# Kernel optimization log

Hardware: AMD Instinct MI355X
Metric: run time of the kernel (lower is better)

## Reference

```python
import jax, jax.numpy as jnp
import numpy as np
import math


def _instance_cl(z1, z2):
    # z1, z2: [B, T, C] -> per-element instance contrastive loss [B, T]
    B = z1.shape[0]
    z = jnp.concatenate([z1, z2], axis=0)          # [2B, T, C]
    z = z.transpose(1, 0, 2)                        # [T, 2B, C]
    sim = jnp.einsum('tic,tjc->tij', z, z)          # [T, 2B, 2B]
    # drop diagonal: tril(-1) shifted + triu(1) shifted -> [T, 2B, 2B-1]
    logits = jnp.tril(sim, -1)[:, :, :-1] + jnp.triu(sim, 1)[:, :, 1:]
    logits = -jax.nn.log_softmax(logits, axis=-1)
    i = jnp.arange(B)
    loss = (logits[:, i, B + i - 1] + logits[:, B + i, i]) / 2.0   # [T, B]
    return loss.T                                    # [B, T]


def _temporal_cl(z1, z2):
    # z1, z2: [B, T, C] -> per-timestep temporal contrastive loss [B, T]
    T = z1.shape[1]
    z = jnp.concatenate([z1, z2], axis=1)            # [B, 2T, C]
    sim = jnp.einsum('bic,bjc->bij', z, z)           # [B, 2T, 2T]
    logits = jnp.tril(sim, -1)[:, :, :-1] + jnp.triu(sim, 1)[:, :, 1:]
    logits = -jax.nn.log_softmax(logits, axis=-1)
    t = jnp.arange(T)
    return (logits[:, t, T + t - 1] + logits[:, T + t, t]) / 2.0   # [B, T]


def _contrastive_corr(z1, z2, alpha=0.5):
    # per-(batch, timestep) contrastive score, shape [B, L]
    return alpha * _instance_cl(z1, z2) + (1.0 - alpha) * _temporal_cl(z1, z2)


def setup_inputs() -> dict:
    key = jax.random.key(0)
    k1, k2, k3 = jax.random.split(key, 3)
    B, L, H, E = 4, 2048, 8, 64
    queries = jax.random.normal(k1, (B, L, H, E), dtype=jnp.float32)
    keys = jax.random.normal(k2, (B, L, H, E), dtype=jnp.float32)
    values = jax.random.normal(k3, (B, L, H, E), dtype=jnp.float32)
    attn_mask = jnp.zeros((1,), dtype=bool)  # unused; ProbMask is rebuilt internally
    return {"queries": queries, "keys": keys, "values": values, "attn_mask": attn_mask}


FACTOR = 1.0


def reference(queries, keys, values, attn_mask):
    B, L, H, E = queries.shape
    # S == L here so key/value slicing branch is a no-op
    corr = _contrastive_corr(queries.reshape(B, L, H * E),
                             keys.reshape(B, L, H * E))       # [B, L]
    top_k = int(FACTOR * math.log(L))                          # static (=7 for L=2048)
    _, index = jax.lax.top_k(corr.mean(axis=0), top_k)         # [K]
    corr_top = corr[:, index]                                  # [B, K]
    # scores[b,h,k,l] = corr_top[b,k] broadcast over h and l
    scores = jnp.broadcast_to(corr_top[:, None, :, None], (B, H, top_k, L))
    # ProbMask: mask future positions l > index[k] (causal for the selected queries)
    mask = jnp.arange(L)[None, :] > index[:, None]             # [K, L]
    scores = jnp.where(mask[None, None, :, :], -jnp.inf, scores)
    attn = jax.nn.softmax(scores, axis=-1)                     # [B, H, K, L]
    V = values.transpose(0, 2, 1, 3)                           # [B, H, L, D]
    context = jnp.cumsum(V, axis=2)                            # initial context (mask_flag=True)
    out = jnp.einsum('bhkl,bhld->bhkd', attn, V)               # [B, H, K, D]
    context = context.at[:, :, index, :].set(out)              # scatter update
    return context
```

## Files before the change

### kernel.cpp

```cpp
#include <hip/hip_runtime.h>
#include <math.h>


typedef __attribute__((ext_vector_type(8))) short short8;
typedef __attribute__((ext_vector_type(8))) unsigned short ushort8;
typedef __attribute__((ext_vector_type(4))) float f32x4;

typedef const __attribute__((address_space(1))) void* gas_ptr;
typedef __attribute__((address_space(3))) void* las_ptr;

#define EXP_OFF 80.0f

__device__ __forceinline__ void async_cp16(const void* g, void* l) {
  __builtin_amdgcn_global_load_lds((gas_ptr)g, (las_ptr)l, 16, 0, 0);
}

__device__ __forceinline__ unsigned short f2bf(float x) {
  union { float f; unsigned int u; } v; v.f = x;
  unsigned int r = v.u + 0x7FFFu + ((v.u >> 16) & 1u);
  return (unsigned short)(r >> 16);
}

__global__ __launch_bounds__(256) void convert_bf16_kernel(
    const float* __restrict__ Q, const float* __restrict__ K,
    unsigned short* __restrict__ Z) {
  int tid = blockIdx.x * 256 + threadIdx.x;
  int row = tid >> 6;
  int c0 = (tid & 63) * 8;
  int b = row >> 12, i = row & 4095;
  const float* src = (i < 2048)
      ? Q + ((size_t)(b * 2048 + i) * 512 + c0)
      : K + ((size_t)(b * 2048 + (i - 2048)) * 512 + c0);
  float4 v0 = ((const float4*)src)[0];
  float4 v1 = ((const float4*)src)[1];
  ushort8 o;
  o[0] = f2bf(v0.x); o[1] = f2bf(v0.y); o[2] = f2bf(v0.z); o[3] = f2bf(v0.w);
  o[4] = f2bf(v1.x); o[5] = f2bf(v1.y); o[6] = f2bf(v1.z); o[7] = f2bf(v1.w);
  *(ushort8*)(Z + (size_t)row * 512 + c0) = o;
}

__global__ __launch_bounds__(256, 3) void temporal_gemm_kernel(
    const unsigned short* __restrict__ Z, float* __restrict__ part,
    float* __restrict__ lse_inst ,
    float* __restrict__ posdot ) {
  __shared__ __align__(16) unsigned short As[2][128 * 32];
  __shared__ __align__(16) unsigned short Bs[2][128 * 32];

  if (blockIdx.x >= 2112) {
    int wave = ((blockIdx.x - 2112) * 256 + threadIdx.x) >> 6;
    int t0 = wave * 2;
    int lane = threadIdx.x & 63;
    int lm = lane & 15, q = lane >> 4;
    int tt = (lm < 8) ? t0 : t0 + 1;
    int v = lm & 7;
    size_t zrow = (v < 4) ? ((size_t)v * 4096 + tt)
                          : ((size_t)(v - 4) * 4096 + 2048 + tt);
    const unsigned short* g = Z + zrow * 512 + q * 8;

    f32x4 acc0 = (f32x4)(0.f), acc1 = (f32x4)(0.f);
#pragma unroll
    for (int kc = 0; kc < 16; kc += 2) {
      short8 a0 = *(const short8*)(g + kc * 32);
      short8 a1 = *(const short8*)(g + kc * 32 + 32);
      acc0 = __builtin_amdgcn_mfma_f32_16x16x32_bf16(a0, a0, acc0, 0, 0, 0);
      acc1 = __builtin_amdgcn_mfma_f32_16x16x32_bf16(a1, a1, acc1, 0, 0, 0);
    }
    f32x4 acc = acc0 + acc1;

#pragma unroll
    for (int rr = 0; rr < 4; rr++) {
      int i = q * 4 + rr;
      float val = acc[rr];
      bool samehalf = ((i < 8) == (lm < 8));
      int t = (i < 8) ? t0 : t0 + 1;
      int iv = i & 7;
      if (samehalf && iv < 4 && (lm & 7) == iv + 4)
        posdot[iv * 2048 + t] = val;
      float dd = (samehalf && lm != i) ? val : -INFINITY;
      float mt = dd;
      mt = fmaxf(mt, __shfl_xor(mt, 1));
      mt = fmaxf(mt, __shfl_xor(mt, 2));
      mt = fmaxf(mt, __shfl_xor(mt, 4));
      float e = __expf(dd - mt);
      e += __shfl_xor(e, 1);
      e += __shfl_xor(e, 2);
      e += __shfl_xor(e, 4);
      if ((lm & 7) == 0 && samehalf) lse_inst[t * 8 + iv] = mt + __logf(e);
    }
    return;
  }

  int id = blockIdx.x;
  int x = id & 7;
  int b = x >> 1;
  int t = (id >> 3) * 2 + (x & 1);
  int cj = (int)((sqrtf(8.0f * (float)t + 1.0f) - 1.0f) * 0.5f);
  while ((cj + 1) * (cj + 2) / 2 <= t) cj++;
  while (cj * (cj + 1) / 2 > t) cj--;
  int ri = t - cj * (cj + 1) / 2;
  const unsigned short* Zb = Z + (size_t)b * 4096 * 512;

  int tid = threadIdx.x;
  int w = tid >> 6, lane = tid & 63;
  int wr = w >> 1, wc = w & 1;
  int lm = lane & 15, q = lane >> 4;
  int swz = q ^ ((lm >> 1) & 3);

  int srow = lane >> 2;
  int kq = (lane & 3) ^ ((lane >> 3) & 3);
  int rl0 = w * 16 + srow;
  int rl1 = 64 + rl0;
  const unsigned short* gA0 = Zb + (size_t)(ri * 128 + rl0) * 512 + kq * 8;
  const unsigned short* gA1 = Zb + (size_t)(ri * 128 + rl1) * 512 + kq * 8;
  const unsigned short* gB0 = Zb + (size_t)(cj * 128 + rl0) * 512 + kq * 8;
  const unsigned short* gB1 = Zb + (size_t)(cj * 128 + rl1) * 512 + kq * 8;
  int lo0 = (w * 16) * 32;
  int lo1 = (64 + w * 16) * 32;

  f32x4 acc[4][4];
#pragma unroll
  for (int mi = 0; mi < 4; mi++)
#pragma unroll
    for (int ni = 0; ni < 4; ni++) acc[mi][ni] = (f32x4)(0.f);

  async_cp16(gA0, As[0] + lo0);
  async_cp16(gA1, As[0] + lo1);
  async_cp16(gB0, Bs[0] + lo0);
  async_cp16(gB1, Bs[0] + lo1);

  for (int kc = 0; kc < 16; ++kc) {
    int cur = kc & 1;
    __syncthreads();

    if (kc < 15) {
      int go = (kc + 1) * 32;
      async_cp16(gA0 + go, As[cur ^ 1] + lo0);
      async_cp16(gA1 + go, As[cur ^ 1] + lo1);
      async_cp16(gB0 + go, Bs[cur ^ 1] + lo0);
      async_cp16(gB1 + go, Bs[cur ^ 1] + lo1);
    }

    short8 af[4], bfr[4];
#pragma unroll
    for (int mi = 0; mi < 4; mi++) {
      int ar = wr * 64 + mi * 16 + lm;
      af[mi] = *(const short8*)(As[cur] + ar * 32 + swz * 8);
    }
#pragma unroll
    for (int ni = 0; ni < 4; ni++) {
      int bc = wc * 64 + ni * 16 + lm;
      bfr[ni] = *(const short8*)(Bs[cur] + bc * 32 + swz * 8);
    }
#pragma unroll
    for (int mi = 0; mi < 4; mi++)
#pragma unroll
      for (int ni = 0; ni < 4; ni++)
        acc[mi][ni] = __builtin_amdgcn_mfma_f32_16x16x32_bf16(
            af[mi], bfr[ni], acc[mi][ni], 0, 0, 0);
  }

  float rsum[4][4];
  float csum[4];
#pragma unroll
  for (int mi = 0; mi < 4; mi++)
#pragma unroll
    for (int rr = 0; rr < 4; rr++) rsum[mi][rr] = 0.f;
#pragma unroll
  for (int ni = 0; ni < 4; ni++) csum[ni] = 0.f;

#pragma unroll
  for (int mi = 0; mi < 4; mi++) {
#pragma unroll
    for (int ni = 0; ni < 4; ni++) {
#pragma unroll
      for (int rr = 0; rr < 4; rr++) {
        int R = ri * 128 + wr * 64 + mi * 16 + q * 4 + rr;
        int Cg = cj * 128 + wc * 64 + ni * 16 + lm;
        float e = (R != Cg) ? __expf(acc[mi][ni][rr] - EXP_OFF) : 0.f;
        rsum[mi][rr] += e;
        csum[ni] += e;
      }
    }
  }

#pragma unroll
  for (int mi = 0; mi < 4; mi++) {
#pragma unroll
    for (int rr = 0; rr < 4; rr++) {
      float s = rsum[mi][rr];
      s += __shfl_xor(s, 1);
      s += __shfl_xor(s, 2);
      s += __shfl_xor(s, 4);
      s += __shfl_xor(s, 8);
      if (lm == 0) {
        int R = ri * 128 + wr * 64 + mi * 16 + q * 4 + rr;
        part[((size_t)(b * 4096 + R)) * 64 + cj * 2 + wc] = s;
      }
    }
  }

  if (ri != cj) {
#pragma unroll
    for (int ni = 0; ni < 4; ni++) {
      float s = csum[ni];
      s += __shfl_xor(s, 16);
      s += __shfl_xor(s, 32);
      if (q == 0) {
        int Cg = cj * 128 + wc * 64 + ni * 16 + lm;
        part[((size_t)(b * 4096 + Cg)) * 64 + ri * 2 + wr] = s;
      }
    }
  }
}

__global__ __launch_bounds__(256) void merge_row_kernel(
    const float* __restrict__ part, float* __restrict__ lse_temp) {
  int row = blockIdx.x * 256 + threadIdx.x;
  const float4* p = (const float4*)(part + (size_t)row * 64);
  float s = 0.f;
#pragma unroll
  for (int i = 0; i < 16; i++) {
    float4 v = p[i];
    s += v.x + v.y + v.z + v.w;
  }
  lse_temp[row] = EXP_OFF + __logf(s);
}

__global__ __launch_bounds__(256) void combine_psum_kernel(
    const float* __restrict__ lse_inst, const float* __restrict__ lse_temp,
    const float* __restrict__ posdot, int* __restrict__ index_out,
    const float* __restrict__ V, float* __restrict__ psum) {
  if (blockIdx.x > 0) {
    int gb = (blockIdx.x - 1) * 4 + (threadIdx.x >> 6);
    int bh = gb >> 6, g = gb & 63;
    int h = bh & 7, b = bh >> 3;
    int lane = threadIdx.x & 63;
    int ro = lane >> 4, e4 = (lane & 15) * 4;
    const float* base =
        V + (size_t)(b * 2048 + g * 32 + ro) * 512 + h * 64 + e4;
    float sx = 0.f, sy = 0.f, sz = 0.f, sw = 0.f;
#pragma unroll
    for (int k = 0; k < 8; k++) {
      float4 v = *(const float4*)(base + (size_t)(k * 4) * 512);
      sx += v.x; sy += v.y; sz += v.z; sw += v.w;
    }
    sx += __shfl_xor(sx, 16); sy += __shfl_xor(sy, 16);
    sz += __shfl_xor(sz, 16); sw += __shfl_xor(sw, 16);
    sx += __shfl_xor(sx, 32); sy += __shfl_xor(sy, 32);
    sz += __shfl_xor(sz, 32); sw += __shfl_xor(sw, 32);
    if (ro == 0) {
      float4 o = {sx, sy, sz, sw};
      *(float4*)(psum + ((size_t)bh * 64 + g) * 64 + e4) = o;
    }
    return;
  }

  __shared__ float wmax[4];
  __shared__ int widx[4];
  int tid = threadIdx.x;
  int base = tid * 8;
  float v[8];
#pragma unroll
  for (int r = 0; r < 8; r++) {
    int t = base + r;
    float sum = 0.f;
#pragma unroll
    for (int b = 0; b < 4; b++) {
      sum += 0.25f * (lse_inst[t * 8 + b] + lse_inst[t * 8 + 4 + b] +
                      lse_temp[b * 4096 + t] + lse_temp[b * 4096 + 2048 + t]) -
             posdot[b * 2048 + t];
    }
    v[r] = sum * 0.25f;
  }
  int lane = tid & 63, w = tid >> 6;
  for (int k = 0; k < 7; k++) {
    float bv = v[0];
    int bi = base;
#pragma unroll
    for (int r = 1; r < 8; r++)
      if (v[r] > bv) { bv = v[r]; bi = base + r; }
#pragma unroll
    for (int d = 1; d < 64; d <<= 1) {
      float ov = __shfl_xor(bv, d);
      int oi = __shfl_xor(bi, d);
      if (ov > bv || (ov == bv && oi < bi)) { bv = ov; bi = oi; }
    }
    if (lane == 0) { wmax[w] = bv; widx[w] = bi; }
    __syncthreads();
    float BV = wmax[0];
    int BI = widx[0];
#pragma unroll
    for (int ww = 1; ww < 4; ww++)
      if (wmax[ww] > BV || (wmax[ww] == BV && widx[ww] < BI)) {
        BV = wmax[ww];
        BI = widx[ww];
      }
    if (tid == 0) index_out[k] = BI;
    if (BI >= base && BI < base + 8) v[BI - base] = -INFINITY;
    __syncthreads();
  }
}

__global__ __launch_bounds__(256) void cumsum_write_kernel(
    const float* __restrict__ V, const float* __restrict__ psum,
    const int* __restrict__ index, float* __restrict__ out) {
  int blk = blockIdx.x;
  int bh = blk >> 4, chunk = blk & 15;
  int h = bh & 7, b = bh >> 3;
  int tid = threadIdx.x;
  int e = tid & 63, sub = tid >> 6;
  int g = chunk * 4 + sub;

  const float* ps = psum + (size_t)bh * 64 * 64;
  float run = 0.f;
  for (int gg = 0; gg < g; ++gg) run += ps[gg * 64 + e];

  int idx[7];
#pragma unroll
  for (int k = 0; k < 7; k++) idx[k] = index[k];

  const float* Vbase = V + (size_t)(b * 2048) * 512 + h * 64 + e;
  float* obase = out + (size_t)bh * 2048 * 64 + e;

  int l0 = g * 32;
#pragma unroll 4
  for (int l = l0; l < l0 + 32; ++l) {
    run += Vbase[(size_t)l * 512];
    float o = run;
    bool special = false;
#pragma unroll
    for (int k = 0; k < 7; k++) special = special || (idx[k] == l);
    if (special) o = run / (float)(l + 1);
    obase[(size_t)l * 64] = o;
  }
}

extern "C" void kernel_launch(void* const* d_in, const int* in_sizes, int n_in,
                              void* d_out, int out_size, void* d_ws, size_t ws_size,
                              hipStream_t stream) {
  const float* Q = (const float*)d_in[0];
  const float* K = (const float*)d_in[1];
  const float* V = (const float*)d_in[2];
  float* out = (float*)d_out;

  unsigned short* Z = (unsigned short*)d_ws;
  float* base = (float*)d_ws + 4 * 4096 * 512 / 2;
  float* part = base;
  float* lse_t = base + 4 * 4096 * 64;
  float* lse_i = lse_t + 16384;
  float* posd = lse_i + 16384;
  int* idx = (int*)(posd + 8192);
  float* psum = part;

  convert_bf16_kernel<<<4096, 256, 0, stream>>>(Q, K, Z);
  temporal_gemm_kernel<<<2368, 256, 0, stream>>>(Z, part, lse_i, posd);
  merge_row_kernel<<<64, 256, 0, stream>>>(part, lse_t);
  combine_psum_kernel<<<513, 256, 0, stream>>>(lse_i, lse_t, posd, idx, V,
                                               psum);
  cumsum_write_kernel<<<512, 256, 0, stream>>>(V, psum, idx, out);
}
```

Before: 188.1 us.

## Triple-buffer GEMM K-loop with prefetch distance two and explicit vmcnt waits

The temporal GEMM's shared-memory staging goes from double to triple buffering, so async global-to-LDS loads are issued two K-chunks ahead. __syncthreads is replaced with an explicit s_waitcnt vmcnt(4) plus s_barrier, so only the oldest stage's loads must finish before each compute step. The aim is to hide more global load latency behind MFMA work. In exchange, LDS per block grows from 32KB to 48KB, which may reduce occupancy against the launch bound of 3 blocks. The hand-written vmcnt also depends on the exact count of outstanding loads.

```diff
diff --git a/kernel.cpp b/kernel.cpp
--- a/kernel.cpp
+++ b/kernel.cpp
@@ -43,8 +43,8 @@
     const unsigned short* __restrict__ Z, float* __restrict__ part,
     float* __restrict__ lse_inst ,
     float* __restrict__ posdot ) {
-  __shared__ __align__(16) unsigned short As[2][128 * 32];
-  __shared__ __align__(16) unsigned short Bs[2][128 * 32];
+  __shared__ __align__(16) unsigned short As[3][128 * 32];
+  __shared__ __align__(16) unsigned short Bs[3][128 * 32];
 
   if (blockIdx.x >= 2112) {
     int wave = ((blockIdx.x - 2112) * 256 + threadIdx.x) >> 6;
@@ -123,33 +123,42 @@
 #pragma unroll
     for (int ni = 0; ni < 4; ni++) acc[mi][ni] = (f32x4)(0.f);
 
-  async_cp16(gA0, As[0] + lo0);
-  async_cp16(gA1, As[0] + lo1);
-  async_cp16(gB0, Bs[0] + lo0);
-  async_cp16(gB1, Bs[0] + lo1);
-
+#define STAGE(kc_, sl_)                                  \
+  do {                                                   \
+    int go_ = (kc_) * 32;                                \
+    async_cp16(gA0 + go_, As[sl_] + lo0);                \
+    async_cp16(gA1 + go_, As[sl_] + lo1);                \
+    async_cp16(gB0 + go_, Bs[sl_] + lo0);                \
+    async_cp16(gB1 + go_, Bs[sl_] + lo1);                \
+  } while (0)
+
+  STAGE(0, 0);
+  STAGE(1, 1);
+
+  int sl = 0;
   for (int kc = 0; kc < 16; ++kc) {
-    int cur = kc & 1;
-    __syncthreads();
-
-    if (kc < 15) {
-      int go = (kc + 1) * 32;
-      async_cp16(gA0 + go, As[cur ^ 1] + lo0);
-      async_cp16(gA1 + go, As[cur ^ 1] + lo1);
-      async_cp16(gB0 + go, Bs[cur ^ 1] + lo0);
-      async_cp16(gB1 + go, Bs[cur ^ 1] + lo1);
+    if (kc < 15)
+      asm volatile("s_waitcnt vmcnt(4)" ::: "memory");
+    else
+      asm volatile("s_waitcnt vmcnt(0)" ::: "memory");
+    asm volatile("s_barrier" ::: "memory");
+
+    if (kc + 2 < 16) {
+      int ss = sl + 2;
+      if (ss >= 3) ss -= 3;
+      STAGE(kc + 2, ss);
     }
 
     short8 af[4], bfr[4];
 #pragma unroll
     for (int mi = 0; mi < 4; mi++) {
       int ar = wr * 64 + mi * 16 + lm;
-      af[mi] = *(const short8*)(As[cur] + ar * 32 + swz * 8);
+      af[mi] = *(const short8*)(As[sl] + ar * 32 + swz * 8);
     }
 #pragma unroll
     for (int ni = 0; ni < 4; ni++) {
       int bc = wc * 64 + ni * 16 + lm;
-      bfr[ni] = *(const short8*)(Bs[cur] + bc * 32 + swz * 8);
+      bfr[ni] = *(const short8*)(Bs[sl] + bc * 32 + swz * 8);
     }
 #pragma unroll
     for (int mi = 0; mi < 4; mi++)
@@ -157,7 +166,10 @@
       for (int ni = 0; ni < 4; ni++)
         acc[mi][ni] = __builtin_amdgcn_mfma_f32_16x16x32_bf16(
             af[mi], bfr[ni], acc[mi][ni], 0, 0, 0);
-  }
+
+    sl = (sl + 1 == 3) ? 0 : sl + 1;
+  }
+#undef STAGE
 
   float rsum[4][4];
   float csum[4];
```

Result: faster. 182.8 us (-2.8%).

## Load GEMM A fragments directly to registers and triple-buffer B tiles in LDS

Applied to the files above, without the earlier changes.

The temporal GEMM main loop stops staging the A tile through LDS. Each wave now loads its A fragments straight from global memory into double-buffered registers, one k-step ahead. The B tile moves to a three-stage LDS ring filled by async global-to-LDS copies two steps ahead, synchronised with explicit vmcnt waits and raw barriers in a fully unrolled loop. This is meant to halve LDS traffic and shared-memory footprint and to deepen prefetch. The trade-offs are more uncoalesced global reads and fragile hand-written wait counts. Separately, the instance-contrastive tail blocks drop from 256 to 192 and use a strided loop to cover the same work.

```diff
diff --git a/kernel.cpp b/kernel.cpp
--- a/kernel.cpp
+++ b/kernel.cpp
@@ -43,49 +43,50 @@
     const unsigned short* __restrict__ Z, float* __restrict__ part,
     float* __restrict__ lse_inst ,
     float* __restrict__ posdot ) {
-  __shared__ __align__(16) unsigned short As[2][128 * 32];
-  __shared__ __align__(16) unsigned short Bs[2][128 * 32];
+  __shared__ __align__(16) unsigned short Bs[3][128 * 32];
 
   if (blockIdx.x >= 2112) {
-    int wave = ((blockIdx.x - 2112) * 256 + threadIdx.x) >> 6;
-    int t0 = wave * 2;
+    int slot = ((blockIdx.x - 2112) * 256 + threadIdx.x) >> 6;
     int lane = threadIdx.x & 63;
     int lm = lane & 15, q = lane >> 4;
-    int tt = (lm < 8) ? t0 : t0 + 1;
     int v = lm & 7;
-    size_t zrow = (v < 4) ? ((size_t)v * 4096 + tt)
-                          : ((size_t)(v - 4) * 4096 + 2048 + tt);
-    const unsigned short* g = Z + zrow * 512 + q * 8;
-
-    f32x4 acc0 = (f32x4)(0.f), acc1 = (f32x4)(0.f);
-#pragma unroll
-    for (int kc = 0; kc < 16; kc += 2) {
-      short8 a0 = *(const short8*)(g + kc * 32);
-      short8 a1 = *(const short8*)(g + kc * 32 + 32);
-      acc0 = __builtin_amdgcn_mfma_f32_16x16x32_bf16(a0, a0, acc0, 0, 0, 0);
-      acc1 = __builtin_amdgcn_mfma_f32_16x16x32_bf16(a1, a1, acc1, 0, 0, 0);
-    }
-    f32x4 acc = acc0 + acc1;
-
-#pragma unroll
-    for (int rr = 0; rr < 4; rr++) {
-      int i = q * 4 + rr;
-      float val = acc[rr];
-      bool samehalf = ((i < 8) == (lm < 8));
-      int t = (i < 8) ? t0 : t0 + 1;
-      int iv = i & 7;
-      if (samehalf && iv < 4 && (lm & 7) == iv + 4)
-        posdot[iv * 2048 + t] = val;
-      float dd = (samehalf && lm != i) ? val : -INFINITY;
-      float mt = dd;
-      mt = fmaxf(mt, __shfl_xor(mt, 1));
-      mt = fmaxf(mt, __shfl_xor(mt, 2));
-      mt = fmaxf(mt, __shfl_xor(mt, 4));
-      float e = __expf(dd - mt);
-      e += __shfl_xor(e, 1);
-      e += __shfl_xor(e, 2);
-      e += __shfl_xor(e, 4);
-      if ((lm & 7) == 0 && samehalf) lse_inst[t * 8 + iv] = mt + __logf(e);
+    for (int wu = slot; wu < 1024; wu += 768) {
+      int t0 = wu * 2;
+      int tt = (lm < 8) ? t0 : t0 + 1;
+      size_t zrow = (v < 4) ? ((size_t)v * 4096 + tt)
+                            : ((size_t)(v - 4) * 4096 + 2048 + tt);
+      const unsigned short* g = Z + zrow * 512 + q * 8;
+
+      f32x4 acc0 = (f32x4)(0.f), acc1 = (f32x4)(0.f);
+#pragma unroll
+      for (int kc = 0; kc < 16; kc += 2) {
+        short8 a0 = *(const short8*)(g + kc * 32);
+        short8 a1 = *(const short8*)(g + kc * 32 + 32);
+        acc0 = __builtin_amdgcn_mfma_f32_16x16x32_bf16(a0, a0, acc0, 0, 0, 0);
+        acc1 = __builtin_amdgcn_mfma_f32_16x16x32_bf16(a1, a1, acc1, 0, 0, 0);
+      }
+      f32x4 acc = acc0 + acc1;
+
+#pragma unroll
+      for (int rr = 0; rr < 4; rr++) {
+        int i = q * 4 + rr;
+        float val = acc[rr];
+        bool samehalf = ((i < 8) == (lm < 8));
+        int t = (i < 8) ? t0 : t0 + 1;
+        int iv = i & 7;
+        if (samehalf && iv < 4 && (lm & 7) == iv + 4)
+          posdot[iv * 2048 + t] = val;
+        float dd = (samehalf && lm != i) ? val : -INFINITY;
+        float mt = dd;
+        mt = fmaxf(mt, __shfl_xor(mt, 1));
+        mt = fmaxf(mt, __shfl_xor(mt, 2));
+        mt = fmaxf(mt, __shfl_xor(mt, 4));
+        float e = __expf(dd - mt);
+        e += __shfl_xor(e, 1);
+        e += __shfl_xor(e, 2);
+        e += __shfl_xor(e, 4);
+        if ((lm & 7) == 0 && samehalf) lse_inst[t * 8 + iv] = mt + __logf(e);
+      }
     }
     return;
   }
@@ -110,54 +111,77 @@
   int kq = (lane & 3) ^ ((lane >> 3) & 3);
   int rl0 = w * 16 + srow;
   int rl1 = 64 + rl0;
-  const unsigned short* gA0 = Zb + (size_t)(ri * 128 + rl0) * 512 + kq * 8;
-  const unsigned short* gA1 = Zb + (size_t)(ri * 128 + rl1) * 512 + kq * 8;
   const unsigned short* gB0 = Zb + (size_t)(cj * 128 + rl0) * 512 + kq * 8;
   const unsigned short* gB1 = Zb + (size_t)(cj * 128 + rl1) * 512 + kq * 8;
   int lo0 = (w * 16) * 32;
   int lo1 = (64 + w * 16) * 32;
 
+  const unsigned short* gAp[4];
+#pragma unroll
+  for (int mi = 0; mi < 4; mi++)
+    gAp[mi] =
+        Zb + (size_t)(ri * 128 + wr * 64 + mi * 16 + lm) * 512 + q * 8;
+
   f32x4 acc[4][4];
 #pragma unroll
   for (int mi = 0; mi < 4; mi++)
 #pragma unroll
     for (int ni = 0; ni < 4; ni++) acc[mi][ni] = (f32x4)(0.f);
 
-  async_cp16(gA0, As[0] + lo0);
-  async_cp16(gA1, As[0] + lo1);
+  short8 af0[4], af1[4];
   async_cp16(gB0, Bs[0] + lo0);
   async_cp16(gB1, Bs[0] + lo1);
-
-  for (int kc = 0; kc < 16; ++kc) {
-    int cur = kc & 1;
-    __syncthreads();
-
-    if (kc < 15) {
-      int go = (kc + 1) * 32;
-      async_cp16(gA0 + go, As[cur ^ 1] + lo0);
-      async_cp16(gA1 + go, As[cur ^ 1] + lo1);
-      async_cp16(gB0 + go, Bs[cur ^ 1] + lo0);
-      async_cp16(gB1 + go, Bs[cur ^ 1] + lo1);
-    }
-
-    short8 af[4], bfr[4];
-#pragma unroll
-    for (int mi = 0; mi < 4; mi++) {
-      int ar = wr * 64 + mi * 16 + lm;
-      af[mi] = *(const short8*)(As[cur] + ar * 32 + swz * 8);
-    }
-#pragma unroll
-    for (int ni = 0; ni < 4; ni++) {
-      int bc = wc * 64 + ni * 16 + lm;
-      bfr[ni] = *(const short8*)(Bs[cur] + bc * 32 + swz * 8);
-    }
-#pragma unroll
-    for (int mi = 0; mi < 4; mi++)
-#pragma unroll
-      for (int ni = 0; ni < 4; ni++)
-        acc[mi][ni] = __builtin_amdgcn_mfma_f32_16x16x32_bf16(
-            af[mi], bfr[ni], acc[mi][ni], 0, 0, 0);
-  }
+  asm volatile("" ::: "memory");
+#pragma unroll
+  for (int mi = 0; mi < 4; mi++) af0[mi] = *(const short8*)(gAp[mi]);
+  asm volatile("" ::: "memory");
+  async_cp16(gB0 + 32, Bs[1] + lo0);
+  async_cp16(gB1 + 32, Bs[1] + lo1);
+
+#define KC_BODY(kc_, AFC, AFN)                                               \
+  {                                                                          \
+    asm volatile("s_waitcnt vmcnt(6)" ::: "memory");                         \
+    asm volatile("s_barrier" ::: "memory");                                  \
+    _Pragma("unroll")                                                        \
+    for (int mi = 0; mi < 4; mi++)                                           \
+      AFN[mi] = *(const short8*)(gAp[mi] + (((kc_) + 1) & 15) * 32);         \
+    {                                                                        \
+      const int bk_ = ((kc_) + 2) & 15;                                      \
+      const int bs_ = ((kc_) + 2) % 3;                                       \
+      async_cp16(gB0 + bk_ * 32, Bs[bs_] + lo0);                             \
+      async_cp16(gB1 + bk_ * 32, Bs[bs_] + lo1);                             \
+    }                                                                        \
+    short8 bfr_[4];                                                          \
+    _Pragma("unroll")                                                        \
+    for (int ni = 0; ni < 4; ni++)                                           \
+      bfr_[ni] = *(const short8*)(Bs[(kc_) % 3] +                            \
+                                  (wc * 64 + ni * 16 + lm) * 32 + swz * 8);  \
+    _Pragma("unroll")                                                        \
+    for (int mi = 0; mi < 4; mi++)                                           \
+      _Pragma("unroll")                                                      \
+      for (int ni = 0; ni < 4; ni++)                                         \
+        acc[mi][ni] = __builtin_amdgcn_mfma_f32_16x16x32_bf16(               \
+            AFC[mi], bfr_[ni], acc[mi][ni], 0, 0, 0);                        \
+  }
+
+  KC_BODY(0, af0, af1)
+  KC_BODY(1, af1, af0)
+  KC_BODY(2, af0, af1)
+  KC_BODY(3, af1, af0)
+  KC_BODY(4, af0, af1)
+  KC_BODY(5, af1, af0)
+  KC_BODY(6, af0, af1)
+  KC_BODY(7, af1, af0)
+  KC_BODY(8, af0, af1)
+  KC_BODY(9, af1, af0)
+  KC_BODY(10, af0, af1)
+  KC_BODY(11, af1, af0)
+  KC_BODY(12, af0, af1)
+  KC_BODY(13, af1, af0)
+  KC_BODY(14, af0, af1)
+  KC_BODY(15, af1, af0)
+#undef KC_BODY
+  asm volatile("s_waitcnt vmcnt(0)" ::: "memory");
 
   float rsum[4][4];
   float csum[4];
@@ -353,7 +377,7 @@
   float* psum = part;
 
   convert_bf16_kernel<<<4096, 256, 0, stream>>>(Q, K, Z);
-  temporal_gemm_kernel<<<2368, 256, 0, stream>>>(Z, part, lse_i, posd);
+  temporal_gemm_kernel<<<2304, 256, 0, stream>>>(Z, part, lse_i, posd);
   merge_row_kernel<<<64, 256, 0, stream>>>(part, lse_t);
   combine_psum_kernel<<<513, 256, 0, stream>>>(lse_i, lse_t, posd, idx, V,
                                                psum);
```

Result: slower. 218.8 us (+16.4%).
